# Optimization experiments

Hardware: AMD Instinct MI355X
Metric: run time of the kernel (lower is better)

Reference implementation:

```python
import jax, jax.numpy as jnp
import numpy as np

MAX_K_QK = 64
MAX_K_V = 64
MAX_K_KNOW = 128


def threshold_gate(scores, tau, max_k):
    # scores: [B,S,N], tau: [B,S,1]
    raw = scores - tau
    gate = jnp.where(raw > 0, raw, 1e-08 * jnp.exp(raw))
    exp_gate = jnp.exp(gate) - 1.0
    k = min(max_k, scores.shape[-1])
    topk_vals, _ = jax.lax.top_k(exp_gate, k)
    threshold = topk_vals[:, :, -1:]
    exp_gate = jnp.where(exp_gate >= threshold, exp_gate, 0.0)
    gate_sum = exp_gate.sum(axis=-1, keepdims=True) + 1e-08
    gate_strength = jnp.tanh(exp_gate.max(axis=-1, keepdims=True))
    return exp_gate / gate_sum * gate_strength


def setup_inputs() -> dict:
    key = jax.random.key(0)
    ks = jax.random.split(key, 8)
    B, S, D = 2, 2048, 1024
    N_QK, N_V, N_KNOW = 4096, 4096, 8192
    scale = 0.02  # keep scores in a sane range for exp()
    return {
        "x": jax.random.normal(ks[0], (B, S, D), jnp.float32),
        "qk_emb": jax.random.normal(ks[1], (N_QK, D), jnp.float32) * scale,
        "v_emb": jax.random.normal(ks[2], (N_V, D), jnp.float32) * scale,
        "know_emb": jax.random.normal(ks[3], (N_KNOW, D), jnp.float32) * scale,
        "w_attn": jax.random.normal(ks[4], (D, 3), jnp.float32) * scale,
        "b_attn": jnp.zeros((3,), jnp.float32),
        "w_know": jax.random.normal(ks[5], (D, 1), jnp.float32) * scale,
        "b_know": jnp.zeros((1,), jnp.float32),
    }


def reference(x, qk_emb, v_emb, know_emb, w_attn, b_attn, w_know, b_know):
    # deterministic=True -> router dropout is identity
    # attention gates
    scores_qk = jnp.einsum("bsd,nd->bsn", x, qk_emb)
    scores_v = jnp.einsum("bsd,nd->bsn", x, v_emb)
    tau_all = x @ w_attn + b_attn  # [B,S,3]
    g_Q = threshold_gate(scores_qk, tau_all[:, :, 0:1], MAX_K_QK)
    g_K = threshold_gate(scores_qk, tau_all[:, :, 1:2], MAX_K_QK)
    g_V = threshold_gate(scores_v, tau_all[:, :, 2:3], MAX_K_V)
    t_qk = 1.0 / qk_emb.shape[0]
    t_v = 1.0 / v_emb.shape[0]
    aux_attn = (
        ((g_Q.mean(axis=(0, 1)) - t_qk) ** 2).sum() * g_Q.shape[-1]
        + ((g_K.mean(axis=(0, 1)) - t_qk) ** 2).sum() * g_K.shape[-1]
        + ((g_V.mean(axis=(0, 1)) - t_v) ** 2).sum() * g_V.shape[-1]
    )
    # knowledge gates
    scores_know = jnp.einsum("bsd,nd->bsn", x, know_emb)
    tau_know = x @ w_know + b_know  # [B,S,1]
    g_know = threshold_gate(scores_know, tau_know, MAX_K_KNOW)
    t_know = 1.0 / know_emb.shape[0]
    aux_know = ((g_know.mean(axis=(0, 1)) - t_know) ** 2).sum() * g_know.shape[-1]
    return (g_Q, g_K, g_V, aux_attn, g_know, aux_know)
```

## Files before the change

### kernel.cpp

```cpp
#include <hip/hip_runtime.h>
#include <hip/hip_bf16.h>


#define M_ROWS 4096
#define DIM    1024
#define N_QK   4096
#define N_KNOW 8192

typedef unsigned short ushortT;
typedef __attribute__((ext_vector_type(8)))  short short8;
typedef __attribute__((ext_vector_type(16))) float f32x16;

__global__ __launch_bounds__(256) void tau_kernel(
    const float* __restrict__ x, const float* __restrict__ w_attn,
    const float* __restrict__ b_attn, const float* __restrict__ w_know,
    const float* __restrict__ b_know, float* __restrict__ tau4, int D)
{
    __shared__ float s_f[4][4];
    const int row = blockIdx.x;
    const int tid = threadIdx.x;
    const float* xr = x + (size_t)row * D;
    float p0 = 0.f, p1 = 0.f, p2 = 0.f, p3 = 0.f;
    for (int d = tid; d < D; d += 256) {
        float xv = xr[d];
        p0 += xv * w_attn[d * 3 + 0];
        p1 += xv * w_attn[d * 3 + 1];
        p2 += xv * w_attn[d * 3 + 2];
        p3 += xv * w_know[d];
    }
#pragma unroll
    for (int o = 32; o > 0; o >>= 1) {
        p0 += __shfl_down(p0, o, 64);
        p1 += __shfl_down(p1, o, 64);
        p2 += __shfl_down(p2, o, 64);
        p3 += __shfl_down(p3, o, 64);
    }
    const int lane = tid & 63, wv = tid >> 6;
    if (lane == 0) { s_f[wv][0] = p0; s_f[wv][1] = p1; s_f[wv][2] = p2; s_f[wv][3] = p3; }
    __syncthreads();
    if (tid < 4) {
        float v = s_f[0][tid] + s_f[1][tid] + s_f[2][tid] + s_f[3][tid];
        v += (tid < 3) ? b_attn[tid] : b_know[0];
        tau4[(size_t)row * 4 + tid] = v;
    }
}

__device__ __forceinline__ void split4(const float4 v, uint2& H, uint2& L) {
    float vv[4] = {v.x, v.y, v.z, v.w};
    unsigned h[4], l[4];
#pragma unroll
    for (int i = 0; i < 4; i++) {
        __hip_bfloat16 hb = __float2bfloat16(vv[i]);
        float r = vv[i] - __bfloat162float(hb);
        __hip_bfloat16 lb = __float2bfloat16(r);
        h[i] = *(ushortT*)&hb;
        l[i] = *(ushortT*)&lb;
    }
    H.x = h[0] | (h[1] << 16); H.y = h[2] | (h[3] << 16);
    L.x = l[0] | (l[1] << 16); L.y = l[2] | (l[3] << 16);
}

__global__ __launch_bounds__(256) void gemm_fused(
    const float* __restrict__ x, const float* __restrict__ qk_emb,
    const float* __restrict__ v_emb, const float* __restrict__ know_emb,
    float* __restrict__ gQ, float* __restrict__ gV, float* __restrict__ gKn)
{
    __shared__ ushortT AH[128 * 32];
    __shared__ ushortT AL[128 * 32];
    __shared__ ushortT BH[128 * 32];
    __shared__ ushortT BL[128 * 32];
    const int tid = threadIdx.x;
    const int wave = tid >> 6, lane = tid & 63;
    const int l32 = lane & 31, h = lane >> 5;
    const int rx3 = l32 & 3;
    const int wm = (wave >> 1) * 64, wn = (wave & 1) * 64;
    const long long m0 = (long long)blockIdx.y * 128;
    const int nblk = blockIdx.x;

    const float* Bsrc; float* C; long long ldc; long long n0;
    if (nblk < 32)      { Bsrc = qk_emb;   C = gQ;  ldc = N_QK;   n0 = (long long)nblk * 128; }
    else if (nblk < 64) { Bsrc = v_emb;    C = gV;  ldc = N_QK;   n0 = (long long)(nblk - 32) * 128; }
    else                { Bsrc = know_emb; C = gKn; ldc = N_KNOW; n0 = (long long)(nblk - 64) * 128; }

    const float* gAp[4]; const float* gBp[4]; int offS[4];
#pragma unroll
    for (int it = 0; it < 4; ++it) {
        int f = it * 256 + tid;
        int r = f >> 3, c4 = f & 7;
        offS[it] = r * 64 + (((c4 >> 1) ^ (r & 3)) << 4) + ((c4 & 1) << 3);
        gAp[it] = x    + (m0 + r) * DIM + c4 * 4;
        gBp[it] = Bsrc + (n0 + r) * DIM + c4 * 4;
    }
    const char* aHp[2]; const char* aLp[2]; const char* bHp[2]; const char* bLp[2];
#pragma unroll
    for (int t = 0; t < 2; ++t) {
        int ra = wm + t * 32 + l32, rb = wn + t * 32 + l32;
        aHp[t] = (const char*)AH + ra * 64;
        aLp[t] = (const char*)AL + ra * 64;
        bHp[t] = (const char*)BH + rb * 64;
        bLp[t] = (const char*)BL + rb * 64;
    }

    f32x16 acc[2][2] = {};
    float4 bufA[4], bufB[4];
#pragma unroll
    for (int it = 0; it < 4; ++it) {
        bufA[it] = *(const float4*)(gAp[it]);
        bufB[it] = *(const float4*)(gBp[it]);
    }

    for (int k0 = 0; k0 < DIM; k0 += 32) {
#pragma unroll
        for (int it = 0; it < 4; ++it) {
            uint2 Hh, Ll;
            split4(bufA[it], Hh, Ll);
            *(uint2*)((char*)AH + offS[it]) = Hh;
            *(uint2*)((char*)AL + offS[it]) = Ll;
            split4(bufB[it], Hh, Ll);
            *(uint2*)((char*)BH + offS[it]) = Hh;
            *(uint2*)((char*)BL + offS[it]) = Ll;
        }
        __syncthreads();
        if (k0 + 32 < DIM) {
#pragma unroll
            for (int it = 0; it < 4; ++it) {
                bufA[it] = *(const float4*)(gAp[it] + k0 + 32);
                bufB[it] = *(const float4*)(gBp[it] + k0 + 32);
            }
        }
#pragma unroll
        for (int kb = 0; kb < 2; ++kb) {
            const int so = ((kb * 2 + h) ^ rx3) * 16;
            short8 aH[2], aL[2], bH[2], bL[2];
#pragma unroll
            for (int t = 0; t < 2; ++t) {
                aH[t] = *(const short8*)(aHp[t] + so);
                aL[t] = *(const short8*)(aLp[t] + so);
                bH[t] = *(const short8*)(bHp[t] + so);
                bL[t] = *(const short8*)(bLp[t] + so);
            }
#pragma unroll
            for (int i = 0; i < 2; ++i)
#pragma unroll
                for (int j = 0; j < 2; ++j) {
                    acc[i][j] = __builtin_amdgcn_mfma_f32_32x32x16_bf16(aH[i], bH[j], acc[i][j], 0, 0, 0);
                    acc[i][j] = __builtin_amdgcn_mfma_f32_32x32x16_bf16(aH[i], bL[j], acc[i][j], 0, 0, 0);
                    acc[i][j] = __builtin_amdgcn_mfma_f32_32x32x16_bf16(aL[i], bH[j], acc[i][j], 0, 0, 0);
                    acc[i][j] = __builtin_amdgcn_mfma_f32_32x32x16_bf16(aL[i], bL[j], acc[i][j], 0, 0, 0);
                }
        }
        __syncthreads();
    }
#pragma unroll
    for (int ti = 0; ti < 2; ++ti)
#pragma unroll
        for (int tj = 0; tj < 2; ++tj) {
            long long col = n0 + wn + tj * 32 + l32;
            long long rb  = m0 + wm + ti * 32 + 4 * h;
#pragma unroll
            for (int reg = 0; reg < 16; ++reg) {
                long long row = rb + (reg & 3) + 8 * (reg >> 2);
                C[row * ldc + col] = acc[ti][tj][reg];
            }
        }
}

__device__ __forceinline__ unsigned floatToKey(float f) {
    unsigned b = __float_as_uint(f);
    return (b & 0x80000000u) ? ~b : (b | 0x80000000u);
}
__device__ __forceinline__ float keyToFloat(unsigned key) {
    unsigned b = (key & 0x80000000u) ? (key & 0x7FFFFFFFu) : ~key;
    return __uint_as_float(b);
}
__device__ __forceinline__ float egate(float raw) {
    float g = raw > 0.f ? raw : 1e-8f * __expf(raw);
    return expf(g) - 1.f;
}

template <int NV, bool VLOAD, bool VSTORE>
__global__ __launch_bounds__(256) void gate_kernel2(
    const float* __restrict__ scores, int N,
    const float* __restrict__ tau4, int tauA, int tauB,
    int ksel, float* __restrict__ outA, float* __restrict__ outB,
    float* __restrict__ colA, float* __restrict__ colB)
{
    __shared__ int s_i[4];
    __shared__ unsigned s_u[4];
    __shared__ float s_f[8];
    const int tid = threadIdx.x, lane = tid & 63, wv = tid >> 6;
    const int row = blockIdx.x;
    const bool hasB = (outB != nullptr);
    const float* srow = scores + (size_t)row * N;

    unsigned keys[NV * 4];
    unsigned kmax = 0u;
#pragma unroll
    for (int i = 0; i < NV; i++) {
        float v0, v1, v2, v3;
        const size_t nb = (size_t)(i * 256 + tid) * 4;
        if (VLOAD) {
            float4 v = *(const float4*)(srow + nb);
            v0 = v.x; v1 = v.y; v2 = v.z; v3 = v.w;
        } else {
            v0 = srow[nb + 0]; v1 = srow[nb + 1];
            v2 = srow[nb + 2]; v3 = srow[nb + 3];
        }
        unsigned a = floatToKey(v0), b = floatToKey(v1);
        unsigned c = floatToKey(v2), d = floatToKey(v3);
        keys[i * 4 + 0] = a; keys[i * 4 + 1] = b;
        keys[i * 4 + 2] = c; keys[i * 4 + 3] = d;
        unsigned m1 = a > b ? a : b, m2 = c > d ? c : d;
        m1 = m1 > m2 ? m1 : m2;
        kmax = kmax > m1 ? kmax : m1;
    }
#pragma unroll
    for (int o = 32; o > 0; o >>= 1) {
        unsigned x = __shfl_down(kmax, o, 64);
        kmax = kmax > x ? kmax : x;
    }
    if (lane == 0) s_u[wv] = kmax;
    __syncthreads();
    { unsigned a = s_u[0], b = s_u[1], c = s_u[2], d = s_u[3];
      unsigned m1 = a > b ? a : b, m2 = c > d ? c : d; kmax = m1 > m2 ? m1 : m2; }
    __syncthreads();

    unsigned lo = 0u, hi = kmax, vk;
    for (;;) {
        if (lo >= hi) { vk = lo; break; }
        unsigned mid = lo + ((hi - lo + 1u) >> 1);
        int c = 0;
#pragma unroll
        for (int i = 0; i < NV * 4; i++) c += (keys[i] >= mid) ? 1 : 0;
#pragma unroll
        for (int o = 32; o > 0; o >>= 1) c += __shfl_down(c, o, 64);
        if (lane == 0) s_i[wv] = c;
        __syncthreads();
        int total = s_i[0] + s_i[1] + s_i[2] + s_i[3];
        __syncthreads();
        if (total == ksel) { vk = mid; break; }
        if (total > ksel) lo = mid; else hi = mid - 1u;
    }

    const float tA = tau4[(size_t)row * 4 + tauA];
    const float tB = hasB ? tau4[(size_t)row * 4 + tauB] : 0.f;
    float sA = 0.f, sB = 0.f;
#pragma unroll
    for (int i = 0; i < NV * 4; i++) {
        if (keys[i] >= vk) {
            float s = keyToFloat(keys[i]);
            sA += egate(s - tA);
            if (hasB) sB += egate(s - tB);
        }
    }
#pragma unroll
    for (int o = 32; o > 0; o >>= 1) {
        sA += __shfl_down(sA, o, 64);
        sB += __shfl_down(sB, o, 64);
    }
    if (lane == 0) { s_f[wv] = sA; s_f[4 + wv] = sB; }
    __syncthreads();
    sA = s_f[0] + s_f[1] + s_f[2] + s_f[3];
    sB = s_f[4] + s_f[5] + s_f[6] + s_f[7];

    const float smax = keyToFloat(kmax);
    const float scaleA = tanhf(egate(smax - tA)) / (sA + 1e-8f);
    const float scaleB = hasB ? tanhf(egate(smax - tB)) / (sB + 1e-8f) : 0.f;

    float* orowA = outA + (size_t)row * N;
    float* orowB = hasB ? outB + (size_t)row * N : nullptr;
#pragma unroll
    for (int i = 0; i < NV; i++) {
        const size_t nb = (size_t)(i * 256 + tid) * 4;
        float ga[4], gb[4];
#pragma unroll
        for (int j = 0; j < 4; j++) {
            unsigned key = keys[i * 4 + j];
            float vA = 0.f, vB = 0.f;
            if (key >= vk) {
                float s = keyToFloat(key);
                vA = egate(s - tA) * scaleA;
                atomicAdd(&colA[nb + j], vA);
                if (hasB) { vB = egate(s - tB) * scaleB; atomicAdd(&colB[nb + j], vB); }
            }
            ga[j] = vA; gb[j] = vB;
        }
        if (VSTORE) {
            *(float4*)(orowA + nb) = make_float4(ga[0], ga[1], ga[2], ga[3]);
            if (hasB) *(float4*)(orowB + nb) = make_float4(gb[0], gb[1], gb[2], gb[3]);
        } else {
#pragma unroll
            for (int j = 0; j < 4; j++) {
                orowA[nb + j] = ga[j];
                if (hasB) orowB[nb + j] = gb[j];
            }
        }
    }
}

__global__ __launch_bounds__(256) void aux_kernel(
    const float* __restrict__ colsum,
    float* __restrict__ auxAttn, float* __restrict__ auxKnow)
{
    __shared__ float s_a[4];
    __shared__ float s_b[4];
    const int tid = threadIdx.x;
    const int lane = tid & 63, wv = tid >> 6;
    const float invM = 1.f / 4096.f;

    float sa = 0.f;
    const float tqk = 1.f / 4096.f;
    for (int i = tid; i < 3 * N_QK; i += 256) {
        float m = colsum[i] * invM - tqk;
        sa += m * m;
    }
    float sk = 0.f;
    const float tkn = 1.f / 8192.f;
    for (int i = tid; i < N_KNOW; i += 256) {
        float m = colsum[3 * N_QK + i] * invM - tkn;
        sk += m * m;
    }
#pragma unroll
    for (int o = 32; o > 0; o >>= 1) {
        sa += __shfl_down(sa, o, 64);
        sk += __shfl_down(sk, o, 64);
    }
    if (lane == 0) { s_a[wv] = sa; s_b[wv] = sk; }
    __syncthreads();
    if (tid == 0) {
        auxAttn[0] = (s_a[0] + s_a[1] + s_a[2] + s_a[3]) * 4096.f;
        auxKnow[0] = (s_b[0] + s_b[1] + s_b[2] + s_b[3]) * 8192.f;
    }
}

extern "C" void kernel_launch(void* const* d_in, const int* in_sizes, int n_in,
                              void* d_out, int out_size, void* d_ws, size_t ws_size,
                              hipStream_t stream)
{
    const float* x        = (const float*)d_in[0];
    const float* qk_emb   = (const float*)d_in[1];
    const float* v_emb    = (const float*)d_in[2];
    const float* know_emb = (const float*)d_in[3];
    const float* w_attn   = (const float*)d_in[4];
    const float* b_attn   = (const float*)d_in[5];
    const float* w_know   = (const float*)d_in[6];
    const float* b_know   = (const float*)d_in[7];
    float* out = (float*)d_out;

    const long long M = M_ROWS;

    float* gQ   = out;
    float* gK   = gQ + (size_t)M * N_QK;
    float* gV   = gK + (size_t)M * N_QK;
    float* auxA = gV + (size_t)M * N_QK;
    float* gKn  = auxA + 1;
    float* auxK = gKn + (size_t)M * N_KNOW;

    float* tau4 = (float*)d_ws;
    float* colsums = tau4 + (size_t)M * 4;
    const long long nColsum = 3 * N_QK + N_KNOW;

    hipMemsetAsync(colsums, 0, nColsum * sizeof(float), stream);
    tau_kernel<<<(int)M, 256, 0, stream>>>(x, w_attn, b_attn, w_know, b_know, tau4, DIM);

    gemm_fused<<<dim3(128, 32), 256, 0, stream>>>(
        x, qk_emb, v_emb, know_emb, gQ, gV, gKn);

    gate_kernel2<4, true, true><<<(int)M, 256, 0, stream>>>(
        gQ, N_QK, tau4, 0, 1, 64, gQ, gK, colsums, colsums + N_QK);
    gate_kernel2<4, true, true><<<(int)M, 256, 0, stream>>>(
        gV, N_QK, tau4, 2, -1, 64, gV, nullptr, colsums + 2 * N_QK, nullptr);
    gate_kernel2<8, false, false><<<(int)M, 256, 0, stream>>>(
        gKn, N_KNOW, tau4, 3, -1, 128, gKn, nullptr, colsums + 3 * N_QK, nullptr);

    aux_kernel<<<1, 256, 0, stream>>>(colsums, auxA, auxK);
}
```

Before: 1.097 ms.

## Pre-split A into bf16 hi/lo, load via global_load_lds, fuse gate kernels

Adds a pre-pass that splits x into interleaved bf16 high/low halves in workspace. The GEMM then streams A straight into LDS with global_load_lds, so the 128 column-blocks no longer each redo the split. The three gate launches are merged into one grid that schedules the long knowledge rows first. The binary-search count buffer is double-buffered to drop one barrier per iteration, and the knowledge gate loads become coalesced strided reads. In exchange it adds workspace traffic for the converted A, possibly chunked by workspace size, plus more launches when the workspace is small.

```diff
diff --git a/kernel.cpp b/kernel.cpp
--- a/kernel.cpp
+++ b/kernel.cpp
@@ -60,19 +60,34 @@
     L.x = l[0] | (l[1] << 16); L.y = l[2] | (l[3] << 16);
 }
 
-__global__ __launch_bounds__(256) void gemm_fused(
-    const float* __restrict__ x, const float* __restrict__ qk_emb,
+__global__ __launch_bounds__(256) void convertA(
+    const float* __restrict__ src, ushortT* __restrict__ dst, int nElem4)
+{
+    int g = blockIdx.x * 256 + threadIdx.x;
+    if (g >= nElem4) return;
+    int row = g >> 8;
+    int c4  = g & 255;
+    int chunk = c4 >> 3, pos = c4 & 7;
+    const float4 v = *(const float4*)(src + (size_t)row * DIM + c4 * 4);
+    uint2 H, L;
+    split4(v, H, L);
+    ushortT* base = dst + (size_t)row * 2048 + chunk * 64;
+    *(uint2*)(base + pos * 4)      = H;
+    *(uint2*)(base + 32 + pos * 4) = L;
+}
+
+__global__ __launch_bounds__(256) void gemm_fused2(
+    const ushortT* __restrict__ Aext, const float* __restrict__ qk_emb,
     const float* __restrict__ v_emb, const float* __restrict__ know_emb,
-    float* __restrict__ gQ, float* __restrict__ gV, float* __restrict__ gKn)
-{
-    __shared__ ushortT AH[128 * 32];
-    __shared__ ushortT AL[128 * 32];
-    __shared__ ushortT BH[128 * 32];
-    __shared__ ushortT BL[128 * 32];
+    float* __restrict__ gQ, float* __restrict__ gV, float* __restrict__ gKn,
+    long long rowOff)
+{
+    __shared__ ushortT AHL[128 * 64];
+    __shared__ ushortT BHL[128 * 64];
     const int tid = threadIdx.x;
     const int wave = tid >> 6, lane = tid & 63;
     const int l32 = lane & 31, h = lane >> 5;
-    const int rx3 = l32 & 3;
+    const int rx7 = l32 & 7;
     const int wm = (wave >> 1) * 64, wn = (wave & 1) * 64;
     const long long m0 = (long long)blockIdx.y * 128;
     const int nblk = blockIdx.x;
@@ -82,62 +97,60 @@
     else if (nblk < 64) { Bsrc = v_emb;    C = gV;  ldc = N_QK;   n0 = (long long)(nblk - 32) * 128; }
     else                { Bsrc = know_emb; C = gKn; ldc = N_KNOW; n0 = (long long)(nblk - 64) * 128; }
 
-    const float* gAp[4]; const float* gBp[4]; int offS[4];
+    const ushortT* gAp[4]; ushortT* lAp[4];
+    const float*   gBp[4]; int offH[4], offL[4];
 #pragma unroll
     for (int it = 0; it < 4; ++it) {
         int f = it * 256 + tid;
-        int r = f >> 3, c4 = f & 7;
-        offS[it] = r * 64 + (((c4 >> 1) ^ (r & 3)) << 4) + ((c4 & 1) << 3);
-        gAp[it] = x    + (m0 + r) * DIM + c4 * 4;
+        int r = f >> 3, sp = f & 7;
+        int sg = sp ^ (r & 7);
+        gAp[it] = Aext + (m0 + r) * 2048 + sg * 8;
+        lAp[it] = AHL + f * 8;
+        int c4 = f & 7;
+        int s = c4 >> 1, hf = c4 & 1;
+        offH[it] = r * 128 + ((s ^ (r & 7)) * 16) + hf * 8;
+        offL[it] = r * 128 + (((4 | s) ^ (r & 7)) * 16) + hf * 8;
         gBp[it] = Bsrc + (n0 + r) * DIM + c4 * 4;
     }
-    const char* aHp[2]; const char* aLp[2]; const char* bHp[2]; const char* bLp[2];
+    const char* pA[2]; const char* pB[2];
 #pragma unroll
     for (int t = 0; t < 2; ++t) {
-        int ra = wm + t * 32 + l32, rb = wn + t * 32 + l32;
-        aHp[t] = (const char*)AH + ra * 64;
-        aLp[t] = (const char*)AL + ra * 64;
-        bHp[t] = (const char*)BH + rb * 64;
-        bLp[t] = (const char*)BL + rb * 64;
+        pA[t] = (const char*)AHL + (wm + t * 32 + l32) * 128;
+        pB[t] = (const char*)BHL + (wn + t * 32 + l32) * 128;
     }
 
     f32x16 acc[2][2] = {};
-    float4 bufA[4], bufB[4];
-#pragma unroll
-    for (int it = 0; it < 4; ++it) {
-        bufA[it] = *(const float4*)(gAp[it]);
-        bufB[it] = *(const float4*)(gBp[it]);
-    }
-
-    for (int k0 = 0; k0 < DIM; k0 += 32) {
+    float4 bufB[4];
+#pragma unroll
+    for (int it = 0; it < 4; ++it) bufB[it] = *(const float4*)(gBp[it]);
+
+    for (int c = 0; c < 32; ++c) {
 #pragma unroll
         for (int it = 0; it < 4; ++it) {
-            uint2 Hh, Ll;
-            split4(bufA[it], Hh, Ll);
-            *(uint2*)((char*)AH + offS[it]) = Hh;
-            *(uint2*)((char*)AL + offS[it]) = Ll;
-            split4(bufB[it], Hh, Ll);
-            *(uint2*)((char*)BH + offS[it]) = Hh;
-            *(uint2*)((char*)BL + offS[it]) = Ll;
+            __builtin_amdgcn_global_load_lds(
+                (const __attribute__((address_space(1))) unsigned*)(const void*)(gAp[it] + c * 64),
+                (__attribute__((address_space(3))) unsigned*)(void*)lAp[it], 16, 0, 0);
+            uint2 H, L;
+            split4(bufB[it], H, L);
+            *(uint2*)((char*)BHL + offH[it]) = H;
+            *(uint2*)((char*)BHL + offL[it]) = L;
         }
         __syncthreads();
-        if (k0 + 32 < DIM) {
-#pragma unroll
-            for (int it = 0; it < 4; ++it) {
-                bufA[it] = *(const float4*)(gAp[it] + k0 + 32);
-                bufB[it] = *(const float4*)(gBp[it] + k0 + 32);
-            }
+        if (c + 1 < 32) {
+#pragma unroll
+            for (int it = 0; it < 4; ++it)
+                bufB[it] = *(const float4*)(gBp[it] + (c + 1) * 32);
         }
 #pragma unroll
         for (int kb = 0; kb < 2; ++kb) {
-            const int so = ((kb * 2 + h) ^ rx3) * 16;
+            const int so = ((kb * 2 + h) ^ rx7) * 16;
             short8 aH[2], aL[2], bH[2], bL[2];
 #pragma unroll
             for (int t = 0; t < 2; ++t) {
-                aH[t] = *(const short8*)(aHp[t] + so);
-                aL[t] = *(const short8*)(aLp[t] + so);
-                bH[t] = *(const short8*)(bHp[t] + so);
-                bL[t] = *(const short8*)(bLp[t] + so);
+                aH[t] = *(const short8*)(pA[t] + so);
+                aL[t] = *(const short8*)(pA[t] + (so ^ 64));
+                bH[t] = *(const short8*)(pB[t] + so);
+                bL[t] = *(const short8*)(pB[t] + (so ^ 64));
             }
 #pragma unroll
             for (int i = 0; i < 2; ++i)
@@ -156,7 +169,7 @@
 #pragma unroll
         for (int tj = 0; tj < 2; ++tj) {
             long long col = n0 + wn + tj * 32 + l32;
-            long long rb  = m0 + wm + ti * 32 + 4 * h;
+            long long rb  = rowOff + m0 + wm + ti * 32 + 4 * h;
 #pragma unroll
             for (int reg = 0; reg < 16; ++reg) {
                 long long row = rb + (reg & 3) + 8 * (reg >> 2);
@@ -179,32 +192,27 @@
 }
 
 template <int NV, bool VLOAD, bool VSTORE>
-__global__ __launch_bounds__(256) void gate_kernel2(
-    const float* __restrict__ scores, int N,
-    const float* __restrict__ tau4, int tauA, int tauB,
-    int ksel, float* __restrict__ outA, float* __restrict__ outB,
-    float* __restrict__ colA, float* __restrict__ colB)
-{
-    __shared__ int s_i[4];
-    __shared__ unsigned s_u[4];
-    __shared__ float s_f[8];
+__device__ __forceinline__ void gate_body(
+    const float* __restrict__ srow, float tA, float tB, bool hasB, int ksel,
+    float* __restrict__ orowA, float* __restrict__ orowB,
+    float* __restrict__ colA, float* __restrict__ colB,
+    int* s_cnt, unsigned* s_u, float* s_f)
+{
     const int tid = threadIdx.x, lane = tid & 63, wv = tid >> 6;
-    const int row = blockIdx.x;
-    const bool hasB = (outB != nullptr);
-    const float* srow = scores + (size_t)row * N;
 
     unsigned keys[NV * 4];
     unsigned kmax = 0u;
 #pragma unroll
     for (int i = 0; i < NV; i++) {
         float v0, v1, v2, v3;
-        const size_t nb = (size_t)(i * 256 + tid) * 4;
         if (VLOAD) {
-            float4 v = *(const float4*)(srow + nb);
+            float4 v = *(const float4*)(srow + (size_t)(i * 256 + tid) * 4);
             v0 = v.x; v1 = v.y; v2 = v.z; v3 = v.w;
         } else {
-            v0 = srow[nb + 0]; v1 = srow[nb + 1];
-            v2 = srow[nb + 2]; v3 = srow[nb + 3];
+            v0 = srow[(i * 4 + 0) * 256 + tid];
+            v1 = srow[(i * 4 + 1) * 256 + tid];
+            v2 = srow[(i * 4 + 2) * 256 + tid];
+            v3 = srow[(i * 4 + 3) * 256 + tid];
         }
         unsigned a = floatToKey(v0), b = floatToKey(v1);
         unsigned c = floatToKey(v2), d = floatToKey(v3);
@@ -223,9 +231,9 @@
     __syncthreads();
     { unsigned a = s_u[0], b = s_u[1], c = s_u[2], d = s_u[3];
       unsigned m1 = a > b ? a : b, m2 = c > d ? c : d; kmax = m1 > m2 ? m1 : m2; }
-    __syncthreads();
 
     unsigned lo = 0u, hi = kmax, vk;
+    int pp = 0;
     for (;;) {
         if (lo >= hi) { vk = lo; break; }
         unsigned mid = lo + ((hi - lo + 1u) >> 1);
@@ -234,16 +242,15 @@
         for (int i = 0; i < NV * 4; i++) c += (keys[i] >= mid) ? 1 : 0;
 #pragma unroll
         for (int o = 32; o > 0; o >>= 1) c += __shfl_down(c, o, 64);
-        if (lane == 0) s_i[wv] = c;
+        if (lane == 0) s_cnt[pp * 4 + wv] = c;
         __syncthreads();
-        int total = s_i[0] + s_i[1] + s_i[2] + s_i[3];
-        __syncthreads();
+        int total = s_cnt[pp * 4 + 0] + s_cnt[pp * 4 + 1]
+                  + s_cnt[pp * 4 + 2] + s_cnt[pp * 4 + 3];
+        pp ^= 1;
         if (total == ksel) { vk = mid; break; }
         if (total > ksel) lo = mid; else hi = mid - 1u;
     }
 
-    const float tA = tau4[(size_t)row * 4 + tauA];
-    const float tB = hasB ? tau4[(size_t)row * 4 + tauB] : 0.f;
     float sA = 0.f, sB = 0.f;
 #pragma unroll
     for (int i = 0; i < NV * 4; i++) {
@@ -267,34 +274,70 @@
     const float scaleA = tanhf(egate(smax - tA)) / (sA + 1e-8f);
     const float scaleB = hasB ? tanhf(egate(smax - tB)) / (sB + 1e-8f) : 0.f;
 
-    float* orowA = outA + (size_t)row * N;
-    float* orowB = hasB ? outB + (size_t)row * N : nullptr;
 #pragma unroll
     for (int i = 0; i < NV; i++) {
-        const size_t nb = (size_t)(i * 256 + tid) * 4;
         float ga[4], gb[4];
+        int eidx[4];
 #pragma unroll
         for (int j = 0; j < 4; j++) {
-            unsigned key = keys[i * 4 + j];
+            int ii = i * 4 + j;
+            int idx = VLOAD ? (i * 1024 + tid * 4 + j) : (ii * 256 + tid);
+            eidx[j] = idx;
+            unsigned key = keys[ii];
             float vA = 0.f, vB = 0.f;
             if (key >= vk) {
                 float s = keyToFloat(key);
                 vA = egate(s - tA) * scaleA;
-                atomicAdd(&colA[nb + j], vA);
-                if (hasB) { vB = egate(s - tB) * scaleB; atomicAdd(&colB[nb + j], vB); }
+                atomicAdd(&colA[idx], vA);
+                if (hasB) { vB = egate(s - tB) * scaleB; atomicAdd(&colB[idx], vB); }
             }
             ga[j] = vA; gb[j] = vB;
         }
         if (VSTORE) {
-            *(float4*)(orowA + nb) = make_float4(ga[0], ga[1], ga[2], ga[3]);
-            if (hasB) *(float4*)(orowB + nb) = make_float4(gb[0], gb[1], gb[2], gb[3]);
+            *(float4*)(orowA + (size_t)eidx[0]) = make_float4(ga[0], ga[1], ga[2], ga[3]);
+            if (hasB) *(float4*)(orowB + (size_t)eidx[0]) = make_float4(gb[0], gb[1], gb[2], gb[3]);
         } else {
 #pragma unroll
             for (int j = 0; j < 4; j++) {
-                orowA[nb + j] = ga[j];
-                if (hasB) orowB[nb + j] = gb[j];
+                orowA[eidx[j]] = ga[j];
+                if (hasB) orowB[eidx[j]] = gb[j];
             }
         }
+    }
+}
+
+__global__ __launch_bounds__(256) void gate_all(
+    const float* __restrict__ tau4,
+    float* __restrict__ gQ, float* __restrict__ gK,
+    float* __restrict__ gV, float* __restrict__ gKn,
+    float* __restrict__ colsums)
+{
+    __shared__ int s_cnt[8];
+    __shared__ unsigned s_u[4];
+    __shared__ float s_f[8];
+    const int bid = blockIdx.x;
+    if (bid < 4096) {
+        const int row = bid;
+        const float t = tau4[(size_t)row * 4 + 3];
+        gate_body<8, false, false>(
+            gKn + (size_t)row * N_KNOW, t, 0.f, false, 128,
+            gKn + (size_t)row * N_KNOW, nullptr,
+            colsums + 3 * N_QK, nullptr, s_cnt, s_u, s_f);
+    } else if (bid < 8192) {
+        const int row = bid - 4096;
+        const float tA = tau4[(size_t)row * 4 + 0];
+        const float tB = tau4[(size_t)row * 4 + 1];
+        gate_body<4, true, true>(
+            gQ + (size_t)row * N_QK, tA, tB, true, 64,
+            gQ + (size_t)row * N_QK, gK + (size_t)row * N_QK,
+            colsums, colsums + N_QK, s_cnt, s_u, s_f);
+    } else {
+        const int row = bid - 8192;
+        const float t = tau4[(size_t)row * 4 + 2];
+        gate_body<4, true, true>(
+            gV + (size_t)row * N_QK, t, 0.f, false, 64,
+            gV + (size_t)row * N_QK, nullptr,
+            colsums + 2 * N_QK, nullptr, s_cnt, s_u, s_f);
     }
 }
 
@@ -356,22 +399,30 @@
     float* gKn  = auxA + 1;
     float* auxK = gKn + (size_t)M * N_KNOW;
 
-    float* tau4 = (float*)d_ws;
+    const long long nColsum = 3 * N_QK + N_KNOW;
+    const long long tail_bytes = (M * 4 + nColsum) * 4;
+    long long tailStart = ((long long)ws_size - tail_bytes) & ~255LL;
+    float* tau4 = (float*)((char*)d_ws + tailStart);
     float* colsums = tau4 + (size_t)M * 4;
-    const long long nColsum = 3 * N_QK + N_KNOW;
+
+    const long long rowB = 4096;
+    long long ra = (tailStart / rowB / 128) * 128;
+    if (ra > M) ra = M;
+    if (ra < 128) ra = 128;
+    ushortT* A_ext = (ushortT*)d_ws;
 
     hipMemsetAsync(colsums, 0, nColsum * sizeof(float), stream);
     tau_kernel<<<(int)M, 256, 0, stream>>>(x, w_attn, b_attn, w_know, b_know, tau4, DIM);
 
-    gemm_fused<<<dim3(128, 32), 256, 0, stream>>>(
-        x, qk_emb, v_emb, know_emb, gQ, gV, gKn);
-
-    gate_kernel2<4, true, true><<<(int)M, 256, 0, stream>>>(
-        gQ, N_QK, tau4, 0, 1, 64, gQ, gK, colsums, colsums + N_QK);
-    gate_kernel2<4, true, true><<<(int)M, 256, 0, stream>>>(
-        gV, N_QK, tau4, 2, -1, 64, gV, nullptr, colsums + 2 * N_QK, nullptr);
-    gate_kernel2<8, false, false><<<(int)M, 256, 0, stream>>>(
-        gKn, N_KNOW, tau4, 3, -1, 128, gKn, nullptr, colsums + 3 * N_QK, nullptr);
+    for (long long a0 = 0; a0 < M; a0 += ra) {
+        long long ac = (M - a0 < ra) ? (M - a0) : ra;
+        int nel4 = (int)(ac * 256);
+        convertA<<<(nel4 + 255) / 256, 256, 0, stream>>>(x + a0 * DIM, A_ext, nel4);
+        gemm_fused2<<<dim3(128, (unsigned)(ac / 128)), 256, 0, stream>>>(
+            A_ext, qk_emb, v_emb, know_emb, gQ, gV, gKn, a0);
+    }
+
+    gate_all<<<12288, 256, 0, stream>>>(tau4, gQ, gK, gV, gKn, colsums);
 
     aux_kernel<<<1, 256, 0, stream>>>(colsums, auxA, auxK);
 }
```

Result: faster. 1.067 ms (-2.7%).
